# Kernel tuning notes

Measured on AMD Instinct MI355X. Metric: run time of the kernel, lower is better.

Reference implementation:

```python
import jax, jax.numpy as jnp
import numpy as np

N = 2_000_000
NUM_PTS = 500_000
NUM_GROUPS = 10_000
NUM_POSITIONS = 8
NUM_CAMS = 8


def _quat_mul(q1, q2):
    """Hamilton product, quaternions stored [x, y, z, w] (pypose convention)."""
    v1, w1 = q1[..., :3], q1[..., 3:4]
    v2, w2 = q2[..., :3], q2[..., 3:4]
    w = w1 * w2 - jnp.sum(v1 * v2, axis=-1, keepdims=True)
    v = w1 * v2 + w2 * v1 + jnp.cross(v1, v2)
    return jnp.concatenate([v, w], axis=-1)


def _quat_rotate(q, p):
    """Rotate points p [...,3] by unit quaternion q [...,4] ([x,y,z,w])."""
    v, w = q[..., :3], q[..., 3:4]
    uv = jnp.cross(v, p)
    uuv = jnp.cross(v, uv)
    return p + 2.0 * (w * uv + uuv)


def _random_se3(key, n, rot_scale=0.1, trans_scale=0.5):
    kq, kt = jax.random.split(key)
    qv = rot_scale * jax.random.normal(kq, (n, 3), dtype=jnp.float32)
    qw = jnp.ones((n, 1), dtype=jnp.float32)
    q = jnp.concatenate([qv, qw], axis=-1)
    q = q / jnp.linalg.norm(q, axis=-1, keepdims=True)
    t = trans_scale * jax.random.normal(kt, (n, 3), dtype=jnp.float32)
    return jnp.concatenate([t, q], axis=-1)  # [n,7] = [tx,ty,tz,qx,qy,qz,qw]


def setup_inputs() -> dict:
    key = jax.random.key(0)
    ks = jax.random.split(key, 10)
    points_2d = 1000.0 * jax.random.uniform(ks[0], (N, 2), dtype=jnp.float32)
    camera_indices = jax.random.randint(ks[1], (N,), 0, NUM_CAMS)
    group_idx = jax.random.randint(ks[2], (N,), 0, NUM_GROUPS)
    member_idx = jax.random.randint(ks[3], (N,), 0, NUM_POSITIONS)
    grouping_indices = jnp.stack([group_idx, member_idx], axis=-1)  # [N,2]
    point_indices = jax.random.randint(ks[4], (N,), 0, NUM_PTS)
    camera_pps = 500.0 + 10.0 * jax.random.normal(ks[5], (NUM_CAMS, 2), dtype=jnp.float32)
    intrs = 1000.0 + 50.0 * jax.random.normal(ks[6], (NUM_CAMS, 2), dtype=jnp.float32)
    # 3D points in front of the rig: z in [4, 10) to keep projection well-conditioned
    xy = 2.0 * jax.random.normal(ks[7], (NUM_PTS, 2), dtype=jnp.float32)
    z = 4.0 + 6.0 * jax.random.uniform(ks[8], (NUM_PTS, 1), dtype=jnp.float32)
    points_3d = jnp.concatenate([xy, z], axis=-1)
    kref, krel = jax.random.split(ks[9])
    ref_poses = _random_se3(kref, NUM_GROUPS)
    rel_poses = _random_se3(krel, NUM_POSITIONS, rot_scale=0.05, trans_scale=0.2)
    return {
        "points_2d": points_2d,
        "camera_indices": camera_indices,
        "grouping_indices": grouping_indices,
        "point_indices": point_indices,
        "camera_pps": camera_pps,
        "intrs": intrs,
        "points_3d": points_3d,
        "ref_poses": ref_poses,
        "rel_poses": rel_poses,
    }


def reference(points_2d, camera_indices, grouping_indices, point_indices,
              camera_pps, intrs, points_3d, ref_poses, rel_poses):
    group_idx = grouping_indices[:, 0]
    member_idx = grouping_indices[:, 1]
    ref = ref_poses[group_idx]    # [N,7]
    rel = rel_poses[member_idx]   # [N,7]
    # SE3 compose: image_pose = rel @ ref  ->  (t_rel + R_rel * t_ref, q_rel * q_ref)
    t = rel[:, :3] + _quat_rotate(rel[:, 3:], ref[:, :3])
    q = _quat_mul(rel[:, 3:], ref[:, 3:])
    # Transform points into camera frame and project (pinhole)
    p_cam = _quat_rotate(q, points_3d[point_indices]) + t  # [N,3]
    uv = intrs[camera_indices] * (p_cam[:, :2] / p_cam[:, 2:3]) + camera_pps[camera_indices]
    return uv - points_2d  # [N,2] reprojection residual
```

## Files before the change

kernel.cpp:

```cpp
#include <hip/hip_runtime.h>


__global__ __launch_bounds__(256) void reproj_kernel(
    const float2* __restrict__ points_2d,
    const int*    __restrict__ camera_indices,
    const int2*   __restrict__ grouping_indices,
    const int*    __restrict__ point_indices,
    const float*  __restrict__ camera_pps,
    const float*  __restrict__ intrs,
    const float*  __restrict__ points_3d,
    const float*  __restrict__ ref_poses,
    const float*  __restrict__ rel_poses,
    float2*       __restrict__ out,
    int n)
{
    __shared__ float s_rel[56];
    __shared__ float s_pps[16];
    __shared__ float s_intr[16];
    int tid = threadIdx.x;
    if (tid < 56) s_rel[tid] = rel_poses[tid];
    if (tid < 16) { s_pps[tid] = camera_pps[tid]; s_intr[tid] = intrs[tid]; }
    __syncthreads();

    int i = blockIdx.x * blockDim.x + tid;
    if (i >= n) return;

    int2  gm  = grouping_indices[i];
    int   pi  = point_indices[i];
    int   cam = camera_indices[i];
    float2 p2d = points_2d[i];

    const float* rp = ref_poses + 7 * gm.x;
    float rtx = rp[0], rty = rp[1], rtz = rp[2];
    float rqx = rp[3], rqy = rp[4], rqz = rp[5], rqw = rp[6];

    const float* lp = s_rel + 7 * gm.y;
    float ltx = lp[0], lty = lp[1], ltz = lp[2];
    float lqx = lp[3], lqy = lp[4], lqz = lp[5], lqw = lp[6];

    float uvx = lqy * rtz - lqz * rty;
    float uvy = lqz * rtx - lqx * rtz;
    float uvz = lqx * rty - lqy * rtx;
    float uuvx = lqy * uvz - lqz * uvy;
    float uuvy = lqz * uvx - lqx * uvz;
    float uuvz = lqx * uvy - lqy * uvx;
    float tx = ltx + rtx + 2.0f * (lqw * uvx + uuvx);
    float ty = lty + rty + 2.0f * (lqw * uvy + uuvy);
    float tz = ltz + rtz + 2.0f * (lqw * uvz + uuvz);

    float qw = lqw * rqw - (lqx * rqx + lqy * rqy + lqz * rqz);
    float qx = lqw * rqx + rqw * lqx + (lqy * rqz - lqz * rqy);
    float qy = lqw * rqy + rqw * lqy + (lqz * rqx - lqx * rqz);
    float qz = lqw * rqz + rqw * lqz + (lqx * rqy - lqy * rqx);

    const float* pp = points_3d + 3 * pi;
    float px = pp[0], py = pp[1], pz = pp[2];

    float v2x = qy * pz - qz * py;
    float v2y = qz * px - qx * pz;
    float v2z = qx * py - qy * px;
    float w2x = qy * v2z - qz * v2y;
    float w2y = qz * v2x - qx * v2z;
    float w2z = qx * v2y - qy * v2x;
    float pcx = px + 2.0f * (qw * v2x + w2x) + tx;
    float pcy = py + 2.0f * (qw * v2y + w2y) + ty;
    float pcz = pz + 2.0f * (qw * v2z + w2z) + tz;

    float invz = 1.0f / pcz;
    float ux = s_intr[2 * cam]     * (pcx * invz) + s_pps[2 * cam];
    float uy = s_intr[2 * cam + 1] * (pcy * invz) + s_pps[2 * cam + 1];

    out[i] = make_float2(ux - p2d.x, uy - p2d.y);
}

extern "C" void kernel_launch(void* const* d_in, const int* in_sizes, int n_in,
                              void* d_out, int out_size, void* d_ws, size_t ws_size,
                              hipStream_t stream) {
    const float2* points_2d       = (const float2*)d_in[0];
    const int*    camera_indices  = (const int*)d_in[1];
    const int2*   grouping        = (const int2*)d_in[2];
    const int*    point_indices   = (const int*)d_in[3];
    const float*  camera_pps      = (const float*)d_in[4];
    const float*  intrs           = (const float*)d_in[5];
    const float*  points_3d       = (const float*)d_in[6];
    const float*  ref_poses       = (const float*)d_in[7];
    const float*  rel_poses       = (const float*)d_in[8];
    float2*       out             = (float2*)d_out;

    int n = in_sizes[1];
    int blocks = (n + 255) / 256;
    reproj_kernel<<<blocks, 256, 0, stream>>>(
        points_2d, camera_indices, grouping, point_indices,
        camera_pps, intrs, points_3d, ref_poses, rel_poses, out, n);
}
```

Baseline: 126.6 us.

## Repack points and ref poses into padded float4 layout for vector gathers

Adds a prep kernel that copies points_3d into a 16-byte-aligned float4 array and ref_poses into 32-byte records in workspace each call. The main kernel then gathers each point with one float4 load and each ref pose with two float4 loads instead of several scalar loads. This reduces gather instruction count and cache-line splits, at the cost of an extra kernel launch and about 6.3 MB of extra read/write traffic per call. It falls back to the original kernel if the workspace is too small.

```diff
diff --git a/kernel.cpp b/kernel.cpp
--- a/kernel.cpp
+++ b/kernel.cpp
@@ -1,5 +1,97 @@
 #include <hip/hip_runtime.h>
 
+
+__global__ __launch_bounds__(256) void prep_kernel(
+    const float* __restrict__ pts3, const float* __restrict__ ref,
+    float* __restrict__ pts4, float* __restrict__ ref8,
+    int npts_dw, int nref_dw)
+{
+    int t = blockIdx.x * blockDim.x + threadIdx.x;
+    if (t < npts_dw) {
+        unsigned q = (unsigned)t / 3u, r = (unsigned)t - 3u * q;
+        pts4[4u * q + r] = pts3[t];
+    } else {
+        int u = t - npts_dw;
+        if (u < nref_dw) {
+            unsigned q = (unsigned)u / 7u, r = (unsigned)u - 7u * q;
+            ref8[8u * q + r] = ref[u];
+        }
+    }
+}
+
+__global__ __launch_bounds__(256) void reproj_fast(
+    const float2* __restrict__ points_2d,
+    const int*    __restrict__ camera_indices,
+    const int2*   __restrict__ grouping_indices,
+    const int*    __restrict__ point_indices,
+    const float*  __restrict__ camera_pps,
+    const float*  __restrict__ intrs,
+    const float4* __restrict__ pts4,
+    const float4* __restrict__ ref8,
+    const float*  __restrict__ rel_poses,
+    float2*       __restrict__ out,
+    int n)
+{
+    __shared__ float s_rel[56];
+    __shared__ float s_pps[16];
+    __shared__ float s_intr[16];
+    int tid = threadIdx.x;
+    if (tid < 56) s_rel[tid] = rel_poses[tid];
+    if (tid < 16) { s_pps[tid] = camera_pps[tid]; s_intr[tid] = intrs[tid]; }
+    __syncthreads();
+
+    int i = blockIdx.x * blockDim.x + tid;
+    if (i >= n) return;
+
+    int2   gm  = grouping_indices[i];
+    int    pi  = point_indices[i];
+    int    cam = camera_indices[i];
+    float2 p2d = points_2d[i];
+
+    float4 pt = pts4[pi];
+    float4 r0 = ref8[2 * gm.x];
+    float4 r1 = ref8[2 * gm.x + 1];
+
+    float rtx = r0.x, rty = r0.y, rtz = r0.z;
+    float rqx = r0.w, rqy = r1.x, rqz = r1.y, rqw = r1.z;
+
+    const float* lp = s_rel + 7 * gm.y;
+    float ltx = lp[0], lty = lp[1], ltz = lp[2];
+    float lqx = lp[3], lqy = lp[4], lqz = lp[5], lqw = lp[6];
+
+    float uvx = lqy * rtz - lqz * rty;
+    float uvy = lqz * rtx - lqx * rtz;
+    float uvz = lqx * rty - lqy * rtx;
+    float uuvx = lqy * uvz - lqz * uvy;
+    float uuvy = lqz * uvx - lqx * uvz;
+    float uuvz = lqx * uvy - lqy * uvx;
+    float tx = ltx + rtx + 2.0f * (lqw * uvx + uuvx);
+    float ty = lty + rty + 2.0f * (lqw * uvy + uuvy);
+    float tz = ltz + rtz + 2.0f * (lqw * uvz + uuvz);
+
+    float qw = lqw * rqw - (lqx * rqx + lqy * rqy + lqz * rqz);
+    float qx = lqw * rqx + rqw * lqx + (lqy * rqz - lqz * rqy);
+    float qy = lqw * rqy + rqw * lqy + (lqz * rqx - lqx * rqz);
+    float qz = lqw * rqz + rqw * lqz + (lqx * rqy - lqy * rqx);
+
+    float px = pt.x, py = pt.y, pz = pt.z;
+
+    float v2x = qy * pz - qz * py;
+    float v2y = qz * px - qx * pz;
+    float v2z = qx * py - qy * px;
+    float w2x = qy * v2z - qz * v2y;
+    float w2y = qz * v2x - qx * v2z;
+    float w2z = qx * v2y - qy * v2x;
+    float pcx = px + 2.0f * (qw * v2x + w2x) + tx;
+    float pcy = py + 2.0f * (qw * v2y + w2y) + ty;
+    float pcz = pz + 2.0f * (qw * v2z + w2z) + tz;
+
+    float invz = 1.0f / pcz;
+    float ux = s_intr[2 * cam]     * (pcx * invz) + s_pps[2 * cam];
+    float uy = s_intr[2 * cam + 1] * (pcy * invz) + s_pps[2 * cam + 1];
+
+    out[i] = make_float2(ux - p2d.x, uy - p2d.y);
+}
 
 __global__ __launch_bounds__(256) void reproj_kernel(
     const float2* __restrict__ points_2d,
@@ -25,9 +117,9 @@
     int i = blockIdx.x * blockDim.x + tid;
     if (i >= n) return;
 
-    int2  gm  = grouping_indices[i];
-    int   pi  = point_indices[i];
-    int   cam = camera_indices[i];
+    int2   gm  = grouping_indices[i];
+    int    pi  = point_indices[i];
+    int    cam = camera_indices[i];
     float2 p2d = points_2d[i];
 
     const float* rp = ref_poses + 7 * gm.x;
@@ -87,9 +179,25 @@
     const float*  rel_poses       = (const float*)d_in[8];
     float2*       out             = (float2*)d_out;
 
-    int n = in_sizes[1];
-    int blocks = (n + 255) / 256;
-    reproj_kernel<<<blocks, 256, 0, stream>>>(
-        points_2d, camera_indices, grouping, point_indices,
-        camera_pps, intrs, points_3d, ref_poses, rel_poses, out, n);
-}
+    int n       = in_sizes[1];
+    int npts    = in_sizes[6] / 3;
+    int ngroups = in_sizes[7] / 7;
+
+    size_t need = (size_t)npts * 16 + (size_t)ngroups * 32;
+    if (ws_size >= need) {
+        float* pts4 = (float*)d_ws;
+        float* ref8 = (float*)((char*)d_ws + (size_t)npts * 16);
+        int npts_dw = npts * 3, nref_dw = ngroups * 7;
+        int total = npts_dw + nref_dw;
+        prep_kernel<<<(total + 255) / 256, 256, 0, stream>>>(
+            points_3d, ref_poses, pts4, ref8, npts_dw, nref_dw);
+        reproj_fast<<<(n + 255) / 256, 256, 0, stream>>>(
+            points_2d, camera_indices, grouping, point_indices,
+            camera_pps, intrs, (const float4*)pts4, (const float4*)ref8,
+            rel_poses, out, n);
+    } else {
+        reproj_kernel<<<(n + 255) / 256, 256, 0, stream>>>(
+            points_2d, camera_indices, grouping, point_indices,
+            camera_pps, intrs, points_3d, ref_poses, rel_poses, out, n);
+    }
+}
```

Measured after the change: 134.8 us. 1.07x slower.

## Repack gather tables to float4 and process four observations per thread

Applied to the files above, without the earlier changes.

Adds a prep kernel that repacks points_3d into 16-byte float4 rows and ref_poses into 32-byte padded rows in workspace, so the random gathers become aligned vector loads. The main kernel now handles four observations per thread, using 128-bit nontemporal loads for the streaming index and 2D-point arrays and nontemporal vector stores for the output. The cost is an extra kernel launch and roughly 8 MB of repacking traffic on every call, plus more registers per thread. It falls back to the original kernel when the workspace is too small.

```diff
diff --git a/kernel.cpp b/kernel.cpp
--- a/kernel.cpp
+++ b/kernel.cpp
@@ -1,5 +1,147 @@
 #include <hip/hip_runtime.h>
 
+
+typedef int   iv4 __attribute__((ext_vector_type(4)));
+typedef float fv4 __attribute__((ext_vector_type(4)));
+
+__global__ __launch_bounds__(256) void prep_kernel(
+    const float* __restrict__ pts3, const float* __restrict__ ref,
+    float4* __restrict__ pts4, float4* __restrict__ ref8,
+    int npts, int ngroups)
+{
+    int t = blockIdx.x * blockDim.x + threadIdx.x;
+    if (t < npts) {
+        const float* p = pts3 + 3 * t;
+        pts4[t] = make_float4(p[0], p[1], p[2], 0.0f);
+    } else {
+        int g = t - npts;
+        if (g < ngroups) {
+            const float* r = ref + 7 * g;
+            ref8[2 * g]     = make_float4(r[0], r[1], r[2], r[3]);
+            ref8[2 * g + 1] = make_float4(r[4], r[5], r[6], 0.0f);
+        }
+    }
+}
+
+__device__ __forceinline__ float2 compute_obs(
+    float px, float py, float pz,
+    const float4& r0, const float4& r1,
+    const float* __restrict__ s_rel,
+    const float* __restrict__ s_intr,
+    const float* __restrict__ s_pps,
+    int gy, int cam, float2 p2d)
+{
+    float rtx = r0.x, rty = r0.y, rtz = r0.z;
+    float rqx = r0.w, rqy = r1.x, rqz = r1.y, rqw = r1.z;
+
+    const float* lp = s_rel + 7 * gy;
+    float ltx = lp[0], lty = lp[1], ltz = lp[2];
+    float lqx = lp[3], lqy = lp[4], lqz = lp[5], lqw = lp[6];
+
+    float uvx = lqy * rtz - lqz * rty;
+    float uvy = lqz * rtx - lqx * rtz;
+    float uvz = lqx * rty - lqy * rtx;
+    float uuvx = lqy * uvz - lqz * uvy;
+    float uuvy = lqz * uvx - lqx * uvz;
+    float uuvz = lqx * uvy - lqy * uvx;
+    float tx = ltx + rtx + 2.0f * (lqw * uvx + uuvx);
+    float ty = lty + rty + 2.0f * (lqw * uvy + uuvy);
+    float tz = ltz + rtz + 2.0f * (lqw * uvz + uuvz);
+
+    float qw = lqw * rqw - (lqx * rqx + lqy * rqy + lqz * rqz);
+    float qx = lqw * rqx + rqw * lqx + (lqy * rqz - lqz * rqy);
+    float qy = lqw * rqy + rqw * lqy + (lqz * rqx - lqx * rqz);
+    float qz = lqw * rqz + rqw * lqz + (lqx * rqy - lqy * rqx);
+
+    float v2x = qy * pz - qz * py;
+    float v2y = qz * px - qx * pz;
+    float v2z = qx * py - qy * px;
+    float w2x = qy * v2z - qz * v2y;
+    float w2y = qz * v2x - qx * v2z;
+    float w2z = qx * v2y - qy * v2x;
+    float pcx = px + 2.0f * (qw * v2x + w2x) + tx;
+    float pcy = py + 2.0f * (qw * v2y + w2y) + ty;
+    float pcz = pz + 2.0f * (qw * v2z + w2z) + tz;
+
+    float invz = 1.0f / pcz;
+    float ux = s_intr[2 * cam]     * (pcx * invz) + s_pps[2 * cam];
+    float uy = s_intr[2 * cam + 1] * (pcy * invz) + s_pps[2 * cam + 1];
+    return make_float2(ux - p2d.x, uy - p2d.y);
+}
+
+__global__ __launch_bounds__(256) void reproj4(
+    const float*  __restrict__ points_2d,
+    const int*    __restrict__ camera_indices,
+    const int*    __restrict__ grouping_indices,
+    const int*    __restrict__ point_indices,
+    const float*  __restrict__ camera_pps,
+    const float*  __restrict__ intrs,
+    const float4* __restrict__ pts4,
+    const float4* __restrict__ ref8,
+    const float*  __restrict__ rel_poses,
+    float*        __restrict__ out,
+    int n)
+{
+    __shared__ float s_rel[56];
+    __shared__ float s_pps[16];
+    __shared__ float s_intr[16];
+    int tid = threadIdx.x;
+    if (tid < 56) s_rel[tid] = rel_poses[tid];
+    if (tid < 16) { s_pps[tid] = camera_pps[tid]; s_intr[tid] = intrs[tid]; }
+    __syncthreads();
+
+    int t = blockIdx.x * blockDim.x + tid;
+    int base = t * 4;
+    if (base >= n) return;
+
+    if (base + 3 < n) {
+        iv4 pi4  = __builtin_nontemporal_load((const iv4*)(point_indices)   + t);
+        iv4 cam4 = __builtin_nontemporal_load((const iv4*)(camera_indices)  + t);
+        iv4 g01  = __builtin_nontemporal_load((const iv4*)(grouping_indices) + 2 * t);
+        iv4 g23  = __builtin_nontemporal_load((const iv4*)(grouping_indices) + 2 * t + 1);
+        fv4 p01  = __builtin_nontemporal_load((const fv4*)(points_2d) + 2 * t);
+        fv4 p23  = __builtin_nontemporal_load((const fv4*)(points_2d) + 2 * t + 1);
+
+        int pis[4] = {pi4.x, pi4.y, pi4.z, pi4.w};
+        int gx[4]  = {g01.x, g01.z, g23.x, g23.z};
+        int gy[4]  = {g01.y, g01.w, g23.y, g23.w};
+        int cm[4]  = {cam4.x, cam4.y, cam4.z, cam4.w};
+        float2 p2d[4] = {make_float2(p01.x, p01.y), make_float2(p01.z, p01.w),
+                         make_float2(p23.x, p23.y), make_float2(p23.z, p23.w)};
+
+        float4 pt[4], r0[4], r1[4];
+#pragma unroll
+        for (int k = 0; k < 4; k++) {
+            pt[k] = pts4[pis[k]];
+            r0[k] = ref8[2 * gx[k]];
+            r1[k] = ref8[2 * gx[k] + 1];
+        }
+
+        float2 res[4];
+#pragma unroll
+        for (int k = 0; k < 4; k++) {
+            res[k] = compute_obs(pt[k].x, pt[k].y, pt[k].z,
+                                 r0[k], r1[k], s_rel, s_intr, s_pps,
+                                 gy[k], cm[k], p2d[k]);
+        }
+
+        fv4 o0 = {res[0].x, res[0].y, res[1].x, res[1].y};
+        fv4 o1 = {res[2].x, res[2].y, res[3].x, res[3].y};
+        __builtin_nontemporal_store(o0, (fv4*)(out) + 2 * t);
+        __builtin_nontemporal_store(o1, (fv4*)(out) + 2 * t + 1);
+    } else {
+        for (int i = base; i < n; i++) {
+            int gxi = grouping_indices[2 * i], gyi = grouping_indices[2 * i + 1];
+            float4 pt = pts4[point_indices[i]];
+            float4 r0 = ref8[2 * gxi];
+            float4 r1 = ref8[2 * gxi + 1];
+            float2 p2d = make_float2(points_2d[2 * i], points_2d[2 * i + 1]);
+            float2 r = compute_obs(pt.x, pt.y, pt.z, r0, r1, s_rel, s_intr, s_pps,
+                                   gyi, camera_indices[i], p2d);
+            out[2 * i] = r.x; out[2 * i + 1] = r.y;
+        }
+    }
+}
 
 __global__ __launch_bounds__(256) void reproj_kernel(
     const float2* __restrict__ points_2d,
@@ -25,71 +167,47 @@
     int i = blockIdx.x * blockDim.x + tid;
     if (i >= n) return;
 
-    int2  gm  = grouping_indices[i];
-    int   pi  = point_indices[i];
-    int   cam = camera_indices[i];
-    float2 p2d = points_2d[i];
-
+    int2 gm = grouping_indices[i];
     const float* rp = ref_poses + 7 * gm.x;
-    float rtx = rp[0], rty = rp[1], rtz = rp[2];
-    float rqx = rp[3], rqy = rp[4], rqz = rp[5], rqw = rp[6];
-
-    const float* lp = s_rel + 7 * gm.y;
-    float ltx = lp[0], lty = lp[1], ltz = lp[2];
-    float lqx = lp[3], lqy = lp[4], lqz = lp[5], lqw = lp[6];
-
-    float uvx = lqy * rtz - lqz * rty;
-    float uvy = lqz * rtx - lqx * rtz;
-    float uvz = lqx * rty - lqy * rtx;
-    float uuvx = lqy * uvz - lqz * uvy;
-    float uuvy = lqz * uvx - lqx * uvz;
-    float uuvz = lqx * uvy - lqy * uvx;
-    float tx = ltx + rtx + 2.0f * (lqw * uvx + uuvx);
-    float ty = lty + rty + 2.0f * (lqw * uvy + uuvy);
-    float tz = ltz + rtz + 2.0f * (lqw * uvz + uuvz);
-
-    float qw = lqw * rqw - (lqx * rqx + lqy * rqy + lqz * rqz);
-    float qx = lqw * rqx + rqw * lqx + (lqy * rqz - lqz * rqy);
-    float qy = lqw * rqy + rqw * lqy + (lqz * rqx - lqx * rqz);
-    float qz = lqw * rqz + rqw * lqz + (lqx * rqy - lqy * rqx);
-
-    const float* pp = points_3d + 3 * pi;
-    float px = pp[0], py = pp[1], pz = pp[2];
-
-    float v2x = qy * pz - qz * py;
-    float v2y = qz * px - qx * pz;
-    float v2z = qx * py - qy * px;
-    float w2x = qy * v2z - qz * v2y;
-    float w2y = qz * v2x - qx * v2z;
-    float w2z = qx * v2y - qy * v2x;
-    float pcx = px + 2.0f * (qw * v2x + w2x) + tx;
-    float pcy = py + 2.0f * (qw * v2y + w2y) + ty;
-    float pcz = pz + 2.0f * (qw * v2z + w2z) + tz;
-
-    float invz = 1.0f / pcz;
-    float ux = s_intr[2 * cam]     * (pcx * invz) + s_pps[2 * cam];
-    float uy = s_intr[2 * cam + 1] * (pcy * invz) + s_pps[2 * cam + 1];
-
-    out[i] = make_float2(ux - p2d.x, uy - p2d.y);
+    float4 r0 = make_float4(rp[0], rp[1], rp[2], rp[3]);
+    float4 r1 = make_float4(rp[4], rp[5], rp[6], 0.0f);
+    const float* pp = points_3d + 3 * point_indices[i];
+    out[i] = compute_obs(pp[0], pp[1], pp[2], r0, r1, s_rel, s_intr, s_pps,
+                         gm.y, camera_indices[i], points_2d[i]);
 }
 
 extern "C" void kernel_launch(void* const* d_in, const int* in_sizes, int n_in,
                               void* d_out, int out_size, void* d_ws, size_t ws_size,
                               hipStream_t stream) {
-    const float2* points_2d       = (const float2*)d_in[0];
+    const float*  points_2d       = (const float*)d_in[0];
     const int*    camera_indices  = (const int*)d_in[1];
-    const int2*   grouping        = (const int2*)d_in[2];
+    const int*    grouping        = (const int*)d_in[2];
     const int*    point_indices   = (const int*)d_in[3];
     const float*  camera_pps      = (const float*)d_in[4];
     const float*  intrs           = (const float*)d_in[5];
     const float*  points_3d       = (const float*)d_in[6];
     const float*  ref_poses       = (const float*)d_in[7];
     const float*  rel_poses       = (const float*)d_in[8];
-    float2*       out             = (float2*)d_out;
-
-    int n = in_sizes[1];
-    int blocks = (n + 255) / 256;
-    reproj_kernel<<<blocks, 256, 0, stream>>>(
-        points_2d, camera_indices, grouping, point_indices,
-        camera_pps, intrs, points_3d, ref_poses, rel_poses, out, n);
-}
+
+    int n       = in_sizes[1];
+    int npts    = in_sizes[6] / 3;
+    int ngroups = in_sizes[7] / 7;
+
+    size_t need = (size_t)npts * 16 + (size_t)ngroups * 32;
+    if (ws_size >= need) {
+        float4* pts4 = (float4*)d_ws;
+        float4* ref8 = (float4*)((char*)d_ws + (size_t)npts * 16);
+        int total = npts + ngroups;
+        prep_kernel<<<(total + 255) / 256, 256, 0, stream>>>(
+            points_3d, ref_poses, pts4, ref8, npts, ngroups);
+        int nt = (n + 3) / 4;
+        reproj4<<<(nt + 255) / 256, 256, 0, stream>>>(
+            points_2d, camera_indices, grouping, point_indices,
+            camera_pps, intrs, pts4, ref8, rel_poses, (float*)d_out, n);
+    } else {
+        reproj_kernel<<<(n + 255) / 256, 256, 0, stream>>>(
+            (const float2*)points_2d, camera_indices, (const int2*)grouping,
+            point_indices, camera_pps, intrs, points_3d, ref_poses, rel_poses,
+            (float2*)d_out, n);
+    }
+}
```

Result: slower. 135.0 us (+6.6%).
